# Kernel tuning notes

Measured on AMD Instinct MI355X. Metric: run time of the kernel, lower is better.

## Reference

```python
import jax, jax.numpy as jnp
import numpy as np

DIM_NODE = 128
DIM_EDGE = 128
DIM_TIME = 100
NUM_HEAD = 8
DIM_OUT = 128
LN_EPS = 1e-5


def setup_inputs() -> dict:
    key = jax.random.key(0)
    ks = jax.random.split(key, 12)
    D, E = 25000, 250000
    src_feat = jax.random.normal(ks[0], (D + E, DIM_NODE), jnp.float32)
    edge_f = jax.random.normal(ks[1], (E, DIM_EDGE), jnp.float32)
    edge_dt = jax.random.uniform(ks[2], (E,), jnp.float32)
    src_idx = jnp.arange(D + E, dtype=jnp.int64)
    edge_dst = jnp.sort(jax.random.randint(ks[3], (E,), 0, D)).astype(jnp.int64)
    # TimeEncode params (fixed init from the module)
    time_w = jnp.asarray(1.0 / 10 ** np.linspace(0, 9, DIM_TIME, dtype=np.float32))  # (DIM_TIME,)
    time_b = jnp.zeros((DIM_TIME,), jnp.float32)
    dq = DIM_NODE + DIM_TIME           # 228
    dkv = DIM_NODE + DIM_EDGE + DIM_TIME  # 356
    s = 0.05
    wq_w = jax.random.normal(ks[4], (DIM_OUT, dq), jnp.float32) * s
    wq_b = jnp.zeros((DIM_OUT,), jnp.float32)
    wk_w = jax.random.normal(ks[5], (DIM_OUT, dkv), jnp.float32) * s
    wk_b = jnp.zeros((DIM_OUT,), jnp.float32)
    wv_w = jax.random.normal(ks[6], (DIM_OUT, dkv), jnp.float32) * s
    wv_b = jnp.zeros((DIM_OUT,), jnp.float32)
    wout_w = jax.random.normal(ks[7], (DIM_OUT, DIM_NODE + DIM_OUT), jnp.float32) * s
    wout_b = jnp.zeros((DIM_OUT,), jnp.float32)
    ln_g = jnp.ones((DIM_OUT,), jnp.float32)
    ln_b = jnp.zeros((DIM_OUT,), jnp.float32)
    return dict(src_feat=src_feat, edge_f=edge_f, edge_dt=edge_dt,
                time_w=time_w, time_b=time_b,
                wq_w=wq_w, wq_b=wq_b, wk_w=wk_w, wk_b=wk_b,
                wv_w=wv_w, wv_b=wv_b, wout_w=wout_w, wout_b=wout_b,
                ln_g=ln_g, ln_b=ln_b, src_idx=src_idx, edge_dst=edge_dst)


def reference(src_feat, edge_f, edge_dt, time_w, time_b,
              wq_w, wq_b, wk_w, wk_b, wv_w, wv_b,
              wout_w, wout_b, ln_g, ln_b, src_idx, edge_dst):
    E = edge_f.shape[0]
    src_data = src_feat[src_idx]              # (D+E, dn)
    D = src_data.shape[0] - E
    q_data = src_data[:D]                     # (D, dn)
    kv_data = src_data[D:]                    # (E, dn)

    # TimeEncode: cos(w * t + b)
    time_feat = jnp.cos(edge_dt[:, None] * time_w[None, :] + time_b)       # (E, dt)
    zero_time_feat = jnp.broadcast_to(jnp.cos(time_b), (D, DIM_TIME))      # (D, dt)

    Qd = jnp.concatenate([q_data, zero_time_feat], axis=1) @ wq_w.T + wq_b  # (D, dout)
    Q = Qd[edge_dst]                                                        # (E, dout)
    kv_in = jnp.concatenate([kv_data, edge_f, time_feat], axis=1)           # (E, dkv)
    K = kv_in @ wk_w.T + wk_b
    V = kv_in @ wv_w.T + wv_b

    dh = DIM_OUT // NUM_HEAD
    Q = Q.reshape(E, NUM_HEAD, dh)
    K = K.reshape(E, NUM_HEAD, dh)
    V = V.reshape(E, NUM_HEAD, dh)

    scores = jax.nn.leaky_relu(jnp.sum(Q * K, axis=2), 0.2)   # (E, H)
    # edge softmax: segment softmax over dst nodes
    m = jax.ops.segment_max(scores, edge_dst, num_segments=D)  # (D, H)
    m = jnp.where(jnp.isfinite(m), m, 0.0)
    ex = jnp.exp(scores - m[edge_dst])
    den = jax.ops.segment_sum(ex, edge_dst, num_segments=D)    # (D, H)
    att = ex / den[edge_dst]                                    # (E, H)

    Vw = (V * att[:, :, None]).reshape(E, DIM_OUT)
    h = jax.ops.segment_sum(Vw, edge_dst, num_segments=D)       # (D, dout)

    rst = jnp.concatenate([h, q_data], axis=1) @ wout_w.T + wout_b
    rst = jax.nn.relu(rst)
    mu = jnp.mean(rst, axis=-1, keepdims=True)
    var = jnp.var(rst, axis=-1, keepdims=True)
    return (rst - mu) / jnp.sqrt(var + LN_EPS) * ln_g + ln_b
```

## Files before the change

### kernel.cpp

```cpp
#include <hip/hip_runtime.h>
#include <stdint.h>

#define DIM_TIME 100
#define DQ 228
#define DKV 356
#define KPAD 384
#define NB 256
#define BM 32
#define BK 32
#define NCHUNK 12
#define A_STRIDE 392
#define C_STRIDE 264

typedef short v8s __attribute__((ext_vector_type(8)));
typedef float v4f __attribute__((ext_vector_type(4)));

__device__ __forceinline__ unsigned short bf16_bits(float f) {
    union { float f; uint32_t u; } c; c.f = f;
    uint32_t u = c.u;
    uint32_t r = (u + 0x7FFFu + ((u >> 16) & 1u)) >> 16;
    return (unsigned short)r;
}
__device__ __forceinline__ float bf16_lo(uint32_t u) {
    union { uint32_t u; float f; } c; c.u = u << 16; return c.f;
}
__device__ __forceinline__ float bf16_hi(uint32_t u) {
    union { uint32_t u; float f; } c; c.u = u & 0xFFFF0000u; return c.f;
}

__global__ void prep_wt2(const float* __restrict__ wk_w, const float* __restrict__ wv_w,
                         unsigned short* __restrict__ Wt2) {
    int n = blockIdx.x;
    int k = threadIdx.x;
    float v = 0.f;
    if (k < DKV) v = (n < 128) ? wk_w[n * DKV + k] : wv_w[(n - 128) * DKV + k];
    Wt2[n * KPAD + k] = bf16_bits(v);
}

__global__ void prep_wqt(const float* __restrict__ wq_w, float* __restrict__ Wqt) {
    int k = blockIdx.x, o = threadIdx.x;
    Wqt[k * 128 + o] = wq_w[o * DQ + k];
}

__global__ void prep_wot(const float* __restrict__ wout_w, float* __restrict__ Wot) {
    int k = blockIdx.x, o = threadIdx.x;
    Wot[k * 128 + o] = wout_w[o * 256 + k];
}

__global__ void prep_cq(const float* __restrict__ wq_w, const float* __restrict__ wq_b,
                        const float* __restrict__ time_b, float* __restrict__ cq) {
    int o = threadIdx.x;
    float s = wq_b[o];
    for (int t = 0; t < DIM_TIME; ++t)
        s += cosf(time_b[t]) * wq_w[o * DQ + 128 + t];
    cq[o] = s;
}

__global__ __launch_bounds__(256) void qd_kernel(
        const float* __restrict__ src_feat, const int* __restrict__ src_idx,
        const float* __restrict__ Wqt, const float* __restrict__ cq,
        float* __restrict__ Qd, int D) {
    __shared__ float q_s[32][128];
    int lane = threadIdx.x & 63, wave = threadIdx.x >> 6;
    int r0 = wave * 8;
    int d0 = blockIdx.x * 32 + r0;
    #pragma unroll
    for (int i = 0; i < 8; ++i) {
        int d = d0 + i;
        float v0 = 0.f, v1 = 0.f;
        if (d < D) {
            const float* p = src_feat + (size_t)src_idx[d] * 128;
            v0 = p[lane]; v1 = p[lane + 64];
        }
        q_s[r0 + i][lane] = v0; q_s[r0 + i][lane + 64] = v1;
    }
    float2 c2 = *(const float2*)(cq + 2 * lane);
    float acc0[8], acc1[8];
    #pragma unroll
    for (int i = 0; i < 8; ++i) { acc0[i] = c2.x; acc1[i] = c2.y; }
    #pragma unroll 8
    for (int k = 0; k < 128; ++k) {
        float2 w = *(const float2*)(Wqt + k * 128 + 2 * lane);
        #pragma unroll
        for (int i = 0; i < 8; ++i) {
            float a = q_s[r0 + i][k];
            acc0[i] += a * w.x; acc1[i] += a * w.y;
        }
    }
    #pragma unroll
    for (int i = 0; i < 8; ++i) {
        int d = d0 + i;
        if (d < D)
            *(float2*)(Qd + (size_t)d * 128 + 2 * lane) = make_float2(acc0[i], acc1[i]);
    }
}

__global__ __launch_bounds__(256) void kv_mfma(
        const float* __restrict__ src_feat, const int* __restrict__ src_idx,
        const float* __restrict__ edge_f, const float* __restrict__ edge_dt,
        const float* __restrict__ time_w, const float* __restrict__ time_b,
        const unsigned short* __restrict__ Wt2,
        const float* __restrict__ wk_b, const float* __restrict__ wv_b,
        unsigned short* __restrict__ KVb, int D, int E) {
    __shared__ unsigned short A_s[BM * A_STRIDE];
    int tid = threadIdx.x;
    int e0 = blockIdx.x * BM;
    int lane = tid & 63, wave = tid >> 6;
    int l15 = lane & 15, quad = lane >> 4;
    int wn = wave * 64;

    {
        int row = tid >> 3;
        int cb  = (tid & 7) * 4;
        int e = e0 + row;
        bool ok = (e < E);
        size_t nbase = ok ? (size_t)src_idx[D + e] * 128 : 0;
        #pragma unroll
        for (int i = 0; i < 4; ++i) {
            int c4 = cb + i;
            float4 v = ok ? *(const float4*)(src_feat + nbase + c4 * 4)
                          : make_float4(0.f, 0.f, 0.f, 0.f);
            ushort4 w;
            w.x = bf16_bits(v.x); w.y = bf16_bits(v.y);
            w.z = bf16_bits(v.z); w.w = bf16_bits(v.w);
            *(ushort4*)&A_s[row * A_STRIDE + c4 * 4] = w;
        }
        #pragma unroll
        for (int i = 0; i < 4; ++i) {
            int c4 = cb + i;
            float4 v = ok ? *(const float4*)(edge_f + (size_t)e * 128 + c4 * 4)
                          : make_float4(0.f, 0.f, 0.f, 0.f);
            ushort4 w;
            w.x = bf16_bits(v.x); w.y = bf16_bits(v.y);
            w.z = bf16_bits(v.z); w.w = bf16_bits(v.w);
            *(ushort4*)&A_s[row * A_STRIDE + 128 + c4 * 4] = w;
        }
    }
    {
        int c = tid & 127;
        int rbase = tid >> 7;
        bool vc = (c < DIM_TIME);
        float tw = vc ? time_w[c] : 0.f;
        float tb = vc ? time_b[c] : 0.f;
        #pragma unroll
        for (int i = 0; i < 16; ++i) {
            int row = i * 2 + rbase;
            int e = e0 + row;
            float v = 0.f;
            if (vc && e < E) v = __cosf(edge_dt[e] * tw + tb);
            A_s[row * A_STRIDE + 256 + c] = bf16_bits(v);
        }
    }
    __syncthreads();

    v4f acc[2][4];
    #pragma unroll
    for (int mf = 0; mf < 2; ++mf)
        #pragma unroll
        for (int nf = 0; nf < 4; ++nf)
            acc[mf][nf] = (v4f)(0.f);

    const unsigned short* wp = Wt2 + (size_t)(wn + l15) * KPAD + quad * 8;
    const unsigned short* ap = A_s + l15 * A_STRIDE + quad * 8;

    v8s bcur[4], acur[2];
    #pragma unroll
    for (int nf = 0; nf < 4; ++nf) bcur[nf] = *(const v8s*)(wp + nf * 16 * KPAD);
    #pragma unroll
    for (int mf = 0; mf < 2; ++mf) acur[mf] = *(const v8s*)(ap + mf * 16 * A_STRIDE);

    #pragma unroll 2
    for (int ch = 0; ch < NCHUNK; ++ch) {
        int k2 = (ch + 1 < NCHUNK) ? (ch + 1) * BK : 0;
        v8s bn[4], an[2];
        #pragma unroll
        for (int nf = 0; nf < 4; ++nf) bn[nf] = *(const v8s*)(wp + nf * 16 * KPAD + k2);
        #pragma unroll
        for (int mf = 0; mf < 2; ++mf) an[mf] = *(const v8s*)(ap + mf * 16 * A_STRIDE + k2);
        #pragma unroll
        for (int mf = 0; mf < 2; ++mf)
            #pragma unroll
            for (int nf = 0; nf < 4; ++nf)
                acc[mf][nf] = __builtin_amdgcn_mfma_f32_16x16x32_bf16(
                                  acur[mf], bcur[nf], acc[mf][nf], 0, 0, 0);
        #pragma unroll
        for (int nf = 0; nf < 4; ++nf) bcur[nf] = bn[nf];
        #pragma unroll
        for (int mf = 0; mf < 2; ++mf) acur[mf] = an[mf];
    }

    __syncthreads();
    #pragma unroll
    for (int nf = 0; nf < 4; ++nf) {
        int n = wn + nf * 16 + l15;
        float bias = (n < 128) ? wk_b[n] : wv_b[n - 128];
        #pragma unroll
        for (int mf = 0; mf < 2; ++mf)
            #pragma unroll
            for (int r = 0; r < 4; ++r)
                A_s[(mf * 16 + quad * 4 + r) * C_STRIDE + n] =
                    bf16_bits(acc[mf][nf][r] + bias);
    }
    __syncthreads();
    #pragma unroll
    for (int j = 0; j < 4; ++j) {
        int c = j * 256 + tid;
        int row = c >> 5;
        int col = (c & 31) * 8;
        if (e0 + row < E) {
            v8s v = *(const v8s*)&A_s[row * C_STRIDE + col];
            *(v8s*)&KVb[(size_t)(e0 + row) * NB + col] = v;
        }
    }
}

__global__ void seg_offsets(const int* __restrict__ edge_dst, int* __restrict__ start,
                            int D, int E) {
    int d = blockIdx.x * blockDim.x + threadIdx.x;
    if (d > D) return;
    int lo = 0, hi = E;
    while (lo < hi) {
        int mid = (lo + hi) >> 1;
        if (edge_dst[mid] < d) lo = mid + 1; else hi = mid;
    }
    start[d] = lo;
}

__global__ __launch_bounds__(256) void attn_kernel(
        const float* __restrict__ Qd, const unsigned short* __restrict__ KVb,
        const int* __restrict__ start, float* __restrict__ h, int D) {
    int lane = threadIdx.x & 63, wave = threadIdx.x >> 6;
    int dbase = blockIdx.x * 16 + wave * 4;
    for (int i = 0; i < 4; ++i) {
        int d = dbase + i;
        if (d >= D) break;
        float2 q = *(const float2*)(Qd + (size_t)d * 128 + lane * 2);
        int s0 = start[d], s1 = start[d + 1];
        float m = -INFINITY, l = 0.f, a0 = 0.f, a1 = 0.f;
        for (int e = s0; e < s1; e += 4) {
            int n = s1 - e; if (n > 4) n = 4;
            uint32_t ku[4], vu[4];
            #pragma unroll
            for (int j = 0; j < 4; ++j) {
                if (j < n) {
                    const unsigned short* kv = KVb + (size_t)(e + j) * 256 + lane * 2;
                    ku[j] = *(const uint32_t*)kv;
                    vu[j] = *(const uint32_t*)(kv + 128);
                }
            }
            for (int j = 0; j < n; ++j) {
                float qk = q.x * bf16_lo(ku[j]) + q.y * bf16_hi(ku[j]);
                qk += __shfl_xor(qk, 4, 8);
                qk += __shfl_xor(qk, 2, 8);
                qk += __shfl_xor(qk, 1, 8);
                float s = qk > 0.f ? qk : 0.2f * qk;
                float nm = fmaxf(m, s);
                float sc = __expf(m - nm);
                float p  = __expf(s - nm);
                l  = l  * sc + p;
                a0 = a0 * sc + p * bf16_lo(vu[j]);
                a1 = a1 * sc + p * bf16_hi(vu[j]);
                m = nm;
            }
        }
        float inv = (l > 0.f) ? 1.f / l : 0.f;
        *(float2*)(h + (size_t)d * 128 + lane * 2) = make_float2(a0 * inv, a1 * inv);
    }
}

__global__ __launch_bounds__(256) void out_kernel(
        const float* __restrict__ h, const float* __restrict__ src_feat,
        const int* __restrict__ src_idx, const float* __restrict__ Wot,
        const float* __restrict__ wout_b, const float* __restrict__ ln_g,
        const float* __restrict__ ln_b, float* __restrict__ out, int D) {
    __shared__ float in_s[32][256];
    int lane = threadIdx.x & 63, wave = threadIdx.x >> 6;
    int r0 = wave * 8;
    int d0 = blockIdx.x * 32 + r0;
    #pragma unroll
    for (int i = 0; i < 8; ++i) {
        int d = d0 + i;
        float a0 = 0.f, a1 = 0.f, b0 = 0.f, b1 = 0.f;
        if (d < D) {
            const float* ph = h + (size_t)d * 128;
            a0 = ph[lane]; a1 = ph[lane + 64];
            const float* pf = src_feat + (size_t)src_idx[d] * 128;
            b0 = pf[lane]; b1 = pf[lane + 64];
        }
        in_s[r0 + i][lane] = a0; in_s[r0 + i][lane + 64] = a1;
        in_s[r0 + i][128 + lane] = b0; in_s[r0 + i][192 + lane] = b1;
    }
    float2 bb = *(const float2*)(wout_b + 2 * lane);
    float acc0[8], acc1[8];
    #pragma unroll
    for (int i = 0; i < 8; ++i) { acc0[i] = bb.x; acc1[i] = bb.y; }
    #pragma unroll 8
    for (int k = 0; k < 256; ++k) {
        float2 w = *(const float2*)(Wot + k * 128 + 2 * lane);
        #pragma unroll
        for (int i = 0; i < 8; ++i) {
            float a = in_s[r0 + i][k];
            acc0[i] += a * w.x; acc1[i] += a * w.y;
        }
    }
    float2 g = *(const float2*)(ln_g + 2 * lane);
    float2 lb = *(const float2*)(ln_b + 2 * lane);
    #pragma unroll
    for (int i = 0; i < 8; ++i) {
        float v0 = fmaxf(acc0[i], 0.f), v1 = fmaxf(acc1[i], 0.f);
        float s1 = v0 + v1, s2 = v0 * v0 + v1 * v1;
        #pragma unroll
        for (int off = 32; off; off >>= 1) {
            s1 += __shfl_xor(s1, off);
            s2 += __shfl_xor(s2, off);
        }
        float mu  = s1 * (1.f / 128.f);
        float var = s2 * (1.f / 128.f) - mu * mu;
        float rs  = rsqrtf(var + 1e-5f);
        int d = d0 + i;
        if (d < D)
            *(float2*)(out + (size_t)d * 128 + 2 * lane) =
                make_float2((v0 - mu) * rs * g.x + lb.x, (v1 - mu) * rs * g.y + lb.y);
    }
}

extern "C" void kernel_launch(void* const* d_in, const int* in_sizes, int n_in,
                              void* d_out, int out_size, void* d_ws, size_t ws_size,
                              hipStream_t stream) {
    const float* src_feat = (const float*)d_in[0];
    const float* edge_f   = (const float*)d_in[1];
    const float* edge_dt  = (const float*)d_in[2];
    const float* time_w   = (const float*)d_in[3];
    const float* time_b   = (const float*)d_in[4];
    const float* wq_w     = (const float*)d_in[5];
    const float* wq_b     = (const float*)d_in[6];
    const float* wk_w     = (const float*)d_in[7];
    const float* wk_b     = (const float*)d_in[8];
    const float* wv_w     = (const float*)d_in[9];
    const float* wv_b     = (const float*)d_in[10];
    const float* wout_w   = (const float*)d_in[11];
    const float* wout_b   = (const float*)d_in[12];
    const float* ln_g     = (const float*)d_in[13];
    const float* ln_b     = (const float*)d_in[14];
    const int*   src_idx  = (const int*)d_in[15];
    const int*   edge_dst = (const int*)d_in[16];

    int DE = in_sizes[0] / 128;
    int E  = in_sizes[1] / 128;
    int D  = DE - E;

    char* ws = (char*)d_ws;
    size_t off = 0;
    auto alloc = [&](size_t bytes) {
        void* p = ws + off;
        off = (off + bytes + 511) & ~(size_t)511;
        return p;
    };
    unsigned short* Wt2   = (unsigned short*)alloc((size_t)NB * KPAD * 2);
    float*          Wqt   = (float*)alloc(128 * 128 * 4);
    float*          Wot   = (float*)alloc(256 * 128 * 4);
    float*          cq    = (float*)alloc(128 * 4);
    float*          Qd    = (float*)alloc((size_t)D * 128 * 4);
    unsigned short* KVb   = (unsigned short*)alloc((size_t)E * 256 * 2);
    float*          hb    = (float*)alloc((size_t)D * 128 * 4);
    int*            start = (int*)alloc((size_t)(D + 1) * 4);

    hipLaunchKernelGGL(prep_wt2, dim3(NB), dim3(KPAD), 0, stream, wk_w, wv_w, Wt2);
    hipLaunchKernelGGL(prep_wqt, dim3(128), dim3(128), 0, stream, wq_w, Wqt);
    hipLaunchKernelGGL(prep_wot, dim3(256), dim3(128), 0, stream, wout_w, Wot);
    hipLaunchKernelGGL(prep_cq, dim3(1), dim3(128), 0, stream, wq_w, wq_b, time_b, cq);
    hipLaunchKernelGGL(qd_kernel, dim3((D + 31) / 32), dim3(256), 0, stream,
                       src_feat, src_idx, Wqt, cq, Qd, D);
    hipLaunchKernelGGL(kv_mfma, dim3((E + BM - 1) / BM), dim3(256), 0, stream,
                       src_feat, src_idx, edge_f, edge_dt, time_w, time_b,
                       Wt2, wk_b, wv_b, KVb, D, E);
    hipLaunchKernelGGL(seg_offsets, dim3((D + 1 + 255) / 256), dim3(256), 0, stream,
                       edge_dst, start, D, E);
    hipLaunchKernelGGL(attn_kernel, dim3((D + 15) / 16), dim3(256), 0, stream,
                       Qd, KVb, start, hb, D);
    hipLaunchKernelGGL(out_kernel, dim3((D + 31) / 32), dim3(256), 0, stream,
                       hb, src_feat, src_idx, Wot, wout_b, ln_g, ln_b, (float*)d_out, D);
}
```

Baseline: 672.8 us.

## Port Q and output projections to bf16 MFMA, stage KV weights in LDS, interleave KV

Replaces the fp32 scalar Q projection and output projection+LayerNorm kernels with bf16 MFMA versions, with weights pre-converted to bf16. The KV GEMM now stages weight chunks through LDS with register double-buffering instead of reading B fragments directly from global memory. K and V are stored interleaved per lane so attention fetches both with one 8-byte load, in batches of 8 edges and with fewer nodes per block. Trades fp32 precision in the Q/out GEMMs for bf16 and adds block barriers in the GEMM loops.

```diff
diff --git a/kernel.cpp b/kernel.cpp
--- a/kernel.cpp
+++ b/kernel.cpp
@@ -10,7 +10,13 @@
 #define BK 32
 #define NCHUNK 12
 #define A_STRIDE 392
+#define BSTR 36
 #define C_STRIDE 264
+
+#define QD_ASTR 136
+#define QD_BSTR 136
+#define OUT_ASTR 264
+#define OUT_CSTR 132
 
 typedef short v8s __attribute__((ext_vector_type(8)));
 typedef float v4f __attribute__((ext_vector_type(4)));
@@ -27,26 +33,30 @@
 __device__ __forceinline__ float bf16_hi(uint32_t u) {
     union { uint32_t u; float f; } c; c.u = u & 0xFFFF0000u; return c.f;
 }
+__device__ __forceinline__ v8s cvt8(float4 a, float4 b) {
+    union { v8s v; unsigned short u[8]; } r;
+    r.u[0] = bf16_bits(a.x); r.u[1] = bf16_bits(a.y);
+    r.u[2] = bf16_bits(a.z); r.u[3] = bf16_bits(a.w);
+    r.u[4] = bf16_bits(b.x); r.u[5] = bf16_bits(b.y);
+    r.u[6] = bf16_bits(b.z); r.u[7] = bf16_bits(b.w);
+    return r.v;
+}
 
 __global__ void prep_wt2(const float* __restrict__ wk_w, const float* __restrict__ wv_w,
                          unsigned short* __restrict__ Wt2) {
-    int n = blockIdx.x;
-    int k = threadIdx.x;
+    int n = blockIdx.x, k = threadIdx.x;
     float v = 0.f;
     if (k < DKV) v = (n < 128) ? wk_w[n * DKV + k] : wv_w[(n - 128) * DKV + k];
     Wt2[n * KPAD + k] = bf16_bits(v);
 }
-
-__global__ void prep_wqt(const float* __restrict__ wq_w, float* __restrict__ Wqt) {
-    int k = blockIdx.x, o = threadIdx.x;
-    Wqt[k * 128 + o] = wq_w[o * DQ + k];
-}
-
-__global__ void prep_wot(const float* __restrict__ wout_w, float* __restrict__ Wot) {
-    int k = blockIdx.x, o = threadIdx.x;
-    Wot[k * 128 + o] = wout_w[o * 256 + k];
-}
-
+__global__ void prep_wqb(const float* __restrict__ wq_w, unsigned short* __restrict__ Wqb) {
+    int n = blockIdx.x, k = threadIdx.x;
+    Wqb[n * 128 + k] = bf16_bits(wq_w[n * DQ + k]);
+}
+__global__ void prep_wob(const float* __restrict__ wout_w, unsigned short* __restrict__ Wob) {
+    int n = blockIdx.x, k = threadIdx.x;
+    Wob[n * 256 + k] = bf16_bits(wout_w[n * 256 + k]);
+}
 __global__ void prep_cq(const float* __restrict__ wq_w, const float* __restrict__ wq_b,
                         const float* __restrict__ time_b, float* __restrict__ cq) {
     int o = threadIdx.x;
@@ -56,42 +66,78 @@
     cq[o] = s;
 }
 
-__global__ __launch_bounds__(256) void qd_kernel(
+__global__ __launch_bounds__(256) void qd_mfma(
         const float* __restrict__ src_feat, const int* __restrict__ src_idx,
-        const float* __restrict__ Wqt, const float* __restrict__ cq,
+        const unsigned short* __restrict__ Wqb, const float* __restrict__ cq,
         float* __restrict__ Qd, int D) {
-    __shared__ float q_s[32][128];
-    int lane = threadIdx.x & 63, wave = threadIdx.x >> 6;
-    int r0 = wave * 8;
-    int d0 = blockIdx.x * 32 + r0;
-    #pragma unroll
-    for (int i = 0; i < 8; ++i) {
-        int d = d0 + i;
-        float v0 = 0.f, v1 = 0.f;
-        if (d < D) {
-            const float* p = src_feat + (size_t)src_idx[d] * 128;
-            v0 = p[lane]; v1 = p[lane + 64];
-        }
-        q_s[r0 + i][lane] = v0; q_s[r0 + i][lane + 64] = v1;
-    }
-    float2 c2 = *(const float2*)(cq + 2 * lane);
-    float acc0[8], acc1[8];
-    #pragma unroll
-    for (int i = 0; i < 8; ++i) { acc0[i] = c2.x; acc1[i] = c2.y; }
-    #pragma unroll 8
-    for (int k = 0; k < 128; ++k) {
-        float2 w = *(const float2*)(Wqt + k * 128 + 2 * lane);
-        #pragma unroll
-        for (int i = 0; i < 8; ++i) {
-            float a = q_s[r0 + i][k];
-            acc0[i] += a * w.x; acc1[i] += a * w.y;
-        }
-    }
-    #pragma unroll
-    for (int i = 0; i < 8; ++i) {
-        int d = d0 + i;
-        if (d < D)
-            *(float2*)(Qd + (size_t)d * 128 + 2 * lane) = make_float2(acc0[i], acc1[i]);
+    __shared__ unsigned short A_s[32 * QD_ASTR];
+    __shared__ unsigned short B_s[128 * QD_BSTR];
+    int tid = threadIdx.x;
+    int lane = tid & 63, wave = tid >> 6;
+    int l15 = lane & 15, quad = lane >> 4;
+    int wn = wave * 32;
+    int d0 = blockIdx.x * 32;
+
+    {
+        int row = tid >> 2, sub = tid & 3;
+        #pragma unroll
+        for (int j = 0; j < 2; ++j) {
+            int r = row + j * 64;
+            #pragma unroll
+            for (int t = 0; t < 4; ++t) {
+                v8s v = *(const v8s*)(Wqb + (size_t)r * 128 + sub * 32 + t * 8);
+                *(v8s*)&B_s[r * QD_BSTR + sub * 32 + t * 8] = v;
+            }
+        }
+    }
+    {
+        int row = tid >> 3, sub = tid & 7;
+        int d = d0 + row;
+        bool ok = (d < D);
+        size_t base = ok ? (size_t)src_idx[d] * 128 : 0;
+        float4 z = make_float4(0.f, 0.f, 0.f, 0.f);
+        float4 f0 = ok ? *(const float4*)(src_feat + base + sub * 16)      : z;
+        float4 f1 = ok ? *(const float4*)(src_feat + base + sub * 16 + 4)  : z;
+        float4 f2 = ok ? *(const float4*)(src_feat + base + sub * 16 + 8)  : z;
+        float4 f3 = ok ? *(const float4*)(src_feat + base + sub * 16 + 12) : z;
+        *(v8s*)&A_s[row * QD_ASTR + sub * 16]     = cvt8(f0, f1);
+        *(v8s*)&A_s[row * QD_ASTR + sub * 16 + 8] = cvt8(f2, f3);
+    }
+    __syncthreads();
+
+    v4f acc[2][2];
+    #pragma unroll
+    for (int mf = 0; mf < 2; ++mf)
+        #pragma unroll
+        for (int nf = 0; nf < 2; ++nf) acc[mf][nf] = (v4f)(0.f);
+
+    #pragma unroll
+    for (int ch = 0; ch < 4; ++ch) {
+        v8s af[2], bf[2];
+        #pragma unroll
+        for (int mf = 0; mf < 2; ++mf)
+            af[mf] = *(const v8s*)&A_s[(mf * 16 + l15) * QD_ASTR + ch * 32 + quad * 8];
+        #pragma unroll
+        for (int nf = 0; nf < 2; ++nf)
+            bf[nf] = *(const v8s*)&B_s[(wn + nf * 16 + l15) * QD_BSTR + ch * 32 + quad * 8];
+        #pragma unroll
+        for (int mf = 0; mf < 2; ++mf)
+            #pragma unroll
+            for (int nf = 0; nf < 2; ++nf)
+                acc[mf][nf] = __builtin_amdgcn_mfma_f32_16x16x32_bf16(
+                                  af[mf], bf[nf], acc[mf][nf], 0, 0, 0);
+    }
+    #pragma unroll
+    for (int nf = 0; nf < 2; ++nf) {
+        int n = wn + nf * 16 + l15;
+        float b = cq[n];
+        #pragma unroll
+        for (int mf = 0; mf < 2; ++mf)
+            #pragma unroll
+            for (int r = 0; r < 4; ++r) {
+                int d = d0 + mf * 16 + quad * 4 + r;
+                if (d < D) Qd[(size_t)d * 128 + n] = acc[mf][nf][r] + b;
+            }
     }
 }
 
@@ -103,37 +149,37 @@
         const float* __restrict__ wk_b, const float* __restrict__ wv_b,
         unsigned short* __restrict__ KVb, int D, int E) {
     __shared__ unsigned short A_s[BM * A_STRIDE];
+    __shared__ unsigned short B_s[NB * BSTR];
     int tid = threadIdx.x;
     int e0 = blockIdx.x * BM;
     int lane = tid & 63, wave = tid >> 6;
     int l15 = lane & 15, quad = lane >> 4;
     int wn = wave * 64;
+    int srow = tid >> 2, ssub = tid & 3;
+    const unsigned short* wsrc = Wt2 + (size_t)srow * KPAD + ssub * 8;
+
+    v8s breg[4];
+    #pragma unroll
+    for (int j = 0; j < 4; ++j)
+        breg[j] = *(const v8s*)(wsrc + (size_t)j * 64 * KPAD);
 
     {
-        int row = tid >> 3;
-        int cb  = (tid & 7) * 4;
+        int row = tid >> 3, cb = (tid & 7) * 4;
         int e = e0 + row;
         bool ok = (e < E);
         size_t nbase = ok ? (size_t)src_idx[D + e] * 128 : 0;
-        #pragma unroll
-        for (int i = 0; i < 4; ++i) {
-            int c4 = cb + i;
-            float4 v = ok ? *(const float4*)(src_feat + nbase + c4 * 4)
-                          : make_float4(0.f, 0.f, 0.f, 0.f);
-            ushort4 w;
-            w.x = bf16_bits(v.x); w.y = bf16_bits(v.y);
-            w.z = bf16_bits(v.z); w.w = bf16_bits(v.w);
-            *(ushort4*)&A_s[row * A_STRIDE + c4 * 4] = w;
-        }
-        #pragma unroll
-        for (int i = 0; i < 4; ++i) {
-            int c4 = cb + i;
-            float4 v = ok ? *(const float4*)(edge_f + (size_t)e * 128 + c4 * 4)
-                          : make_float4(0.f, 0.f, 0.f, 0.f);
-            ushort4 w;
-            w.x = bf16_bits(v.x); w.y = bf16_bits(v.y);
-            w.z = bf16_bits(v.z); w.w = bf16_bits(v.w);
-            *(ushort4*)&A_s[row * A_STRIDE + 128 + c4 * 4] = w;
+        float4 z = make_float4(0.f, 0.f, 0.f, 0.f);
+        #pragma unroll
+        for (int i = 0; i < 4; i += 2) {
+            float4 a = ok ? *(const float4*)(src_feat + nbase + (cb + i) * 4)     : z;
+            float4 b = ok ? *(const float4*)(src_feat + nbase + (cb + i + 1) * 4) : z;
+            *(v8s*)&A_s[row * A_STRIDE + (cb + i) * 4] = cvt8(a, b);
+        }
+        #pragma unroll
+        for (int i = 0; i < 4; i += 2) {
+            float4 a = ok ? *(const float4*)(edge_f + (size_t)e * 128 + (cb + i) * 4)     : z;
+            float4 b = ok ? *(const float4*)(edge_f + (size_t)e * 128 + (cb + i + 1) * 4) : z;
+            *(v8s*)&A_s[row * A_STRIDE + 128 + (cb + i) * 4] = cvt8(a, b);
         }
     }
     {
@@ -152,53 +198,60 @@
         }
     }
     __syncthreads();
+    #pragma unroll
+    for (int j = 0; j < 4; ++j)
+        *(v8s*)&B_s[(srow + j * 64) * BSTR + ssub * 8] = breg[j];
+    #pragma unroll
+    for (int j = 0; j < 4; ++j)
+        breg[j] = *(const v8s*)(wsrc + (size_t)j * 64 * KPAD + BK);
+    __syncthreads();
 
     v4f acc[2][4];
     #pragma unroll
     for (int mf = 0; mf < 2; ++mf)
         #pragma unroll
+        for (int nf = 0; nf < 4; ++nf) acc[mf][nf] = (v4f)(0.f);
+
+    for (int ch = 0; ch < NCHUNK; ++ch) {
+        v8s af[2], bf[4];
+        #pragma unroll
+        for (int mf = 0; mf < 2; ++mf)
+            af[mf] = *(const v8s*)&A_s[(mf * 16 + l15) * A_STRIDE + ch * BK + quad * 8];
+        #pragma unroll
         for (int nf = 0; nf < 4; ++nf)
-            acc[mf][nf] = (v4f)(0.f);
-
-    const unsigned short* wp = Wt2 + (size_t)(wn + l15) * KPAD + quad * 8;
-    const unsigned short* ap = A_s + l15 * A_STRIDE + quad * 8;
-
-    v8s bcur[4], acur[2];
-    #pragma unroll
-    for (int nf = 0; nf < 4; ++nf) bcur[nf] = *(const v8s*)(wp + nf * 16 * KPAD);
-    #pragma unroll
-    for (int mf = 0; mf < 2; ++mf) acur[mf] = *(const v8s*)(ap + mf * 16 * A_STRIDE);
-
-    #pragma unroll 2
-    for (int ch = 0; ch < NCHUNK; ++ch) {
-        int k2 = (ch + 1 < NCHUNK) ? (ch + 1) * BK : 0;
-        v8s bn[4], an[2];
-        #pragma unroll
-        for (int nf = 0; nf < 4; ++nf) bn[nf] = *(const v8s*)(wp + nf * 16 * KPAD + k2);
-        #pragma unroll
-        for (int mf = 0; mf < 2; ++mf) an[mf] = *(const v8s*)(ap + mf * 16 * A_STRIDE + k2);
+            bf[nf] = *(const v8s*)&B_s[(wn + nf * 16 + l15) * BSTR + quad * 8];
         #pragma unroll
         for (int mf = 0; mf < 2; ++mf)
             #pragma unroll
             for (int nf = 0; nf < 4; ++nf)
                 acc[mf][nf] = __builtin_amdgcn_mfma_f32_16x16x32_bf16(
-                                  acur[mf], bcur[nf], acc[mf][nf], 0, 0, 0);
-        #pragma unroll
-        for (int nf = 0; nf < 4; ++nf) bcur[nf] = bn[nf];
-        #pragma unroll
-        for (int mf = 0; mf < 2; ++mf) acur[mf] = an[mf];
+                                  af[mf], bf[nf], acc[mf][nf], 0, 0, 0);
+        if (ch + 1 < NCHUNK) {
+            __syncthreads();
+            #pragma unroll
+            for (int j = 0; j < 4; ++j)
+                *(v8s*)&B_s[(srow + j * 64) * BSTR + ssub * 8] = breg[j];
+            if (ch + 2 < NCHUNK) {
+                #pragma unroll
+                for (int j = 0; j < 4; ++j)
+                    breg[j] = *(const v8s*)(wsrc + (size_t)j * 64 * KPAD + (ch + 2) * BK);
+            }
+            __syncthreads();
+        }
     }
 
     __syncthreads();
     #pragma unroll
     for (int nf = 0; nf < 4; ++nf) {
         int n = wn + nf * 16 + l15;
-        float bias = (n < 128) ? wk_b[n] : wv_b[n - 128];
+        float bias; int slot;
+        if (n < 128) { bias = wk_b[n]; slot = 2 * n - (n & 1); }
+        else { int m = n - 128; bias = wv_b[m]; slot = 2 * m + 2 - (m & 1); }
         #pragma unroll
         for (int mf = 0; mf < 2; ++mf)
             #pragma unroll
             for (int r = 0; r < 4; ++r)
-                A_s[(mf * 16 + quad * 4 + r) * C_STRIDE + n] =
+                A_s[(mf * 16 + quad * 4 + r) * C_STRIDE + slot] =
                     bf16_bits(acc[mf][nf][r] + bias);
     }
     __syncthreads();
@@ -230,26 +283,25 @@
         const float* __restrict__ Qd, const unsigned short* __restrict__ KVb,
         const int* __restrict__ start, float* __restrict__ h, int D) {
     int lane = threadIdx.x & 63, wave = threadIdx.x >> 6;
-    int dbase = blockIdx.x * 16 + wave * 4;
-    for (int i = 0; i < 4; ++i) {
+    int dbase = blockIdx.x * 8 + wave * 2;
+    #pragma unroll
+    for (int i = 0; i < 2; ++i) {
         int d = dbase + i;
-        if (d >= D) break;
+        if (d >= D) continue;
         float2 q = *(const float2*)(Qd + (size_t)d * 128 + lane * 2);
         int s0 = start[d], s1 = start[d + 1];
         float m = -INFINITY, l = 0.f, a0 = 0.f, a1 = 0.f;
-        for (int e = s0; e < s1; e += 4) {
-            int n = s1 - e; if (n > 4) n = 4;
-            uint32_t ku[4], vu[4];
-            #pragma unroll
-            for (int j = 0; j < 4; ++j) {
-                if (j < n) {
-                    const unsigned short* kv = KVb + (size_t)(e + j) * 256 + lane * 2;
-                    ku[j] = *(const uint32_t*)kv;
-                    vu[j] = *(const uint32_t*)(kv + 128);
-                }
+        for (int e = s0; e < s1; e += 8) {
+            int n = s1 - e; if (n > 8) n = 8;
+            uint2 w8[8];
+            #pragma unroll
+            for (int j = 0; j < 8; ++j) {
+                int idx = e + j; if (idx >= s1) idx = s1 - 1;
+                w8[j] = *(const uint2*)(KVb + (size_t)idx * 256 + lane * 4);
             }
             for (int j = 0; j < n; ++j) {
-                float qk = q.x * bf16_lo(ku[j]) + q.y * bf16_hi(ku[j]);
+                uint32_t ku = w8[j].x, vu = w8[j].y;
+                float qk = q.x * bf16_lo(ku) + q.y * bf16_hi(ku);
                 qk += __shfl_xor(qk, 4, 8);
                 qk += __shfl_xor(qk, 2, 8);
                 qk += __shfl_xor(qk, 1, 8);
@@ -258,8 +310,8 @@
                 float sc = __expf(m - nm);
                 float p  = __expf(s - nm);
                 l  = l  * sc + p;
-                a0 = a0 * sc + p * bf16_lo(vu[j]);
-                a1 = a1 * sc + p * bf16_hi(vu[j]);
+                a0 = a0 * sc + p * bf16_lo(vu);
+                a1 = a1 * sc + p * bf16_hi(vu);
                 m = nm;
             }
         }
@@ -268,59 +320,148 @@
     }
 }
 
-__global__ __launch_bounds__(256) void out_kernel(
+__global__ __launch_bounds__(256) void out_mfma(
         const float* __restrict__ h, const float* __restrict__ src_feat,
-        const int* __restrict__ src_idx, const float* __restrict__ Wot,
+        const int* __restrict__ src_idx, const unsigned short* __restrict__ Wob,
         const float* __restrict__ wout_b, const float* __restrict__ ln_g,
         const float* __restrict__ ln_b, float* __restrict__ out, int D) {
-    __shared__ float in_s[32][256];
-    int lane = threadIdx.x & 63, wave = threadIdx.x >> 6;
-    int r0 = wave * 8;
-    int d0 = blockIdx.x * 32 + r0;
-    #pragma unroll
-    for (int i = 0; i < 8; ++i) {
-        int d = d0 + i;
-        float a0 = 0.f, a1 = 0.f, b0 = 0.f, b1 = 0.f;
-        if (d < D) {
-            const float* ph = h + (size_t)d * 128;
-            a0 = ph[lane]; a1 = ph[lane + 64];
-            const float* pf = src_feat + (size_t)src_idx[d] * 128;
-            b0 = pf[lane]; b1 = pf[lane + 64];
-        }
-        in_s[r0 + i][lane] = a0; in_s[r0 + i][lane + 64] = a1;
-        in_s[r0 + i][128 + lane] = b0; in_s[r0 + i][192 + lane] = b1;
-    }
-    float2 bb = *(const float2*)(wout_b + 2 * lane);
-    float acc0[8], acc1[8];
-    #pragma unroll
-    for (int i = 0; i < 8; ++i) { acc0[i] = bb.x; acc1[i] = bb.y; }
-    #pragma unroll 8
-    for (int k = 0; k < 256; ++k) {
-        float2 w = *(const float2*)(Wot + k * 128 + 2 * lane);
-        #pragma unroll
-        for (int i = 0; i < 8; ++i) {
-            float a = in_s[r0 + i][k];
-            acc0[i] += a * w.x; acc1[i] += a * w.y;
-        }
-    }
-    float2 g = *(const float2*)(ln_g + 2 * lane);
-    float2 lb = *(const float2*)(ln_b + 2 * lane);
-    #pragma unroll
-    for (int i = 0; i < 8; ++i) {
-        float v0 = fmaxf(acc0[i], 0.f), v1 = fmaxf(acc1[i], 0.f);
-        float s1 = v0 + v1, s2 = v0 * v0 + v1 * v1;
-        #pragma unroll
-        for (int off = 32; off; off >>= 1) {
-            s1 += __shfl_xor(s1, off);
-            s2 += __shfl_xor(s2, off);
-        }
+    __shared__ unsigned short A_s[32 * OUT_ASTR];
+    __shared__ unsigned short B_s[128 * BSTR];
+    __shared__ float C_s[32 * OUT_CSTR];
+    int tid = threadIdx.x;
+    int lane = tid & 63, wave = tid >> 6;
+    int l15 = lane & 15, quad = lane >> 4;
+    int wn = wave * 32;
+    int d0 = blockIdx.x * 32;
+    int srow = tid >> 2, ssub = tid & 3;
+    const unsigned short* wsrc = Wob + (size_t)srow * 256 + ssub * 8;
+
+    v8s breg[2];
+    #pragma unroll
+    for (int j = 0; j < 2; ++j)
+        breg[j] = *(const v8s*)(wsrc + (size_t)j * 64 * 256);
+
+    {
+        int row = tid >> 3, sub = tid & 7;
+        int d = d0 + row;
+        bool ok = (d < D);
+        const float* src = (sub < 4) ? (ok ? h + (size_t)d * 128 + sub * 32 : h)
+                                     : (ok ? src_feat + (size_t)src_idx[d] * 128 + (sub - 4) * 32
+                                           : src_feat);
+        float4 z = make_float4(0.f, 0.f, 0.f, 0.f);
+        float4 f0 = ok ? *(const float4*)(src)      : z;
+        float4 f1 = ok ? *(const float4*)(src + 4)  : z;
+        float4 f2 = ok ? *(const float4*)(src + 8)  : z;
+        float4 f3 = ok ? *(const float4*)(src + 12) : z;
+        float4 f4 = ok ? *(const float4*)(src + 16) : z;
+        float4 f5 = ok ? *(const float4*)(src + 20) : z;
+        float4 f6 = ok ? *(const float4*)(src + 24) : z;
+        float4 f7 = ok ? *(const float4*)(src + 28) : z;
+        *(v8s*)&A_s[row * OUT_ASTR + sub * 32]      = cvt8(f0, f1);
+        *(v8s*)&A_s[row * OUT_ASTR + sub * 32 + 8]  = cvt8(f2, f3);
+        *(v8s*)&A_s[row * OUT_ASTR + sub * 32 + 16] = cvt8(f4, f5);
+        *(v8s*)&A_s[row * OUT_ASTR + sub * 32 + 24] = cvt8(f6, f7);
+    }
+    __syncthreads();
+    #pragma unroll
+    for (int j = 0; j < 2; ++j)
+        *(v8s*)&B_s[(srow + j * 64) * BSTR + ssub * 8] = breg[j];
+    #pragma unroll
+    for (int j = 0; j < 2; ++j)
+        breg[j] = *(const v8s*)(wsrc + (size_t)j * 64 * 256 + BK);
+    __syncthreads();
+
+    v4f acc[2][2];
+    #pragma unroll
+    for (int mf = 0; mf < 2; ++mf)
+        #pragma unroll
+        for (int nf = 0; nf < 2; ++nf) acc[mf][nf] = (v4f)(0.f);
+
+    for (int ch = 0; ch < 8; ++ch) {
+        v8s af[2], bf[2];
+        #pragma unroll
+        for (int mf = 0; mf < 2; ++mf)
+            af[mf] = *(const v8s*)&A_s[(mf * 16 + l15) * OUT_ASTR + ch * BK + quad * 8];
+        #pragma unroll
+        for (int nf = 0; nf < 2; ++nf)
+            bf[nf] = *(const v8s*)&B_s[(wn + nf * 16 + l15) * BSTR + quad * 8];
+        #pragma unroll
+        for (int mf = 0; mf < 2; ++mf)
+            #pragma unroll
+            for (int nf = 0; nf < 2; ++nf)
+                acc[mf][nf] = __builtin_amdgcn_mfma_f32_16x16x32_bf16(
+                                  af[mf], bf[nf], acc[mf][nf], 0, 0, 0);
+        if (ch + 1 < 8) {
+            __syncthreads();
+            #pragma unroll
+            for (int j = 0; j < 2; ++j)
+                *(v8s*)&B_s[(srow + j * 64) * BSTR + ssub * 8] = breg[j];
+            if (ch + 2 < 8) {
+                #pragma unroll
+                for (int j = 0; j < 2; ++j)
+                    breg[j] = *(const v8s*)(wsrc + (size_t)j * 64 * 256 + (ch + 2) * BK);
+            }
+            __syncthreads();
+        }
+    }
+
+    __syncthreads();
+    #pragma unroll
+    for (int nf = 0; nf < 2; ++nf) {
+        int n = wn + nf * 16 + l15;
+        float b = wout_b[n];
+        #pragma unroll
+        for (int mf = 0; mf < 2; ++mf)
+            #pragma unroll
+            for (int r = 0; r < 4; ++r)
+                C_s[(mf * 16 + quad * 4 + r) * OUT_CSTR + n] =
+                    fmaxf(acc[mf][nf][r] + b, 0.f);
+    }
+    __syncthreads();
+
+    {
+        int row = tid >> 3, s = tid & 7;
+        const float* cr = C_s + row * OUT_CSTR + s * 16;
+        float4 x0 = *(const float4*)(cr);
+        float4 x1 = *(const float4*)(cr + 4);
+        float4 x2 = *(const float4*)(cr + 8);
+        float4 x3 = *(const float4*)(cr + 12);
+        float s1 = x0.x+x0.y+x0.z+x0.w + x1.x+x1.y+x1.z+x1.w
+                 + x2.x+x2.y+x2.z+x2.w + x3.x+x3.y+x3.z+x3.w;
+        float s2 = x0.x*x0.x+x0.y*x0.y+x0.z*x0.z+x0.w*x0.w
+                 + x1.x*x1.x+x1.y*x1.y+x1.z*x1.z+x1.w*x1.w
+                 + x2.x*x2.x+x2.y*x2.y+x2.z*x2.z+x2.w*x2.w
+                 + x3.x*x3.x+x3.y*x3.y+x3.z*x3.z+x3.w*x3.w;
+        s1 += __shfl_xor(s1, 4, 8); s2 += __shfl_xor(s2, 4, 8);
+        s1 += __shfl_xor(s1, 2, 8); s2 += __shfl_xor(s2, 2, 8);
+        s1 += __shfl_xor(s1, 1, 8); s2 += __shfl_xor(s2, 1, 8);
         float mu  = s1 * (1.f / 128.f);
         float var = s2 * (1.f / 128.f) - mu * mu;
         float rs  = rsqrtf(var + 1e-5f);
-        int d = d0 + i;
-        if (d < D)
-            *(float2*)(out + (size_t)d * 128 + 2 * lane) =
-                make_float2((v0 - mu) * rs * g.x + lb.x, (v1 - mu) * rs * g.y + lb.y);
+        int d = d0 + row;
+        if (d < D) {
+            float4 g0 = *(const float4*)(ln_g + s * 16);
+            float4 g1 = *(const float4*)(ln_g + s * 16 + 4);
+            float4 g2 = *(const float4*)(ln_g + s * 16 + 8);
+            float4 g3 = *(const float4*)(ln_g + s * 16 + 12);
+            float4 b0 = *(const float4*)(ln_b + s * 16);
+            float4 b1 = *(const float4*)(ln_b + s * 16 + 4);
+            float4 b2 = *(const float4*)(ln_b + s * 16 + 8);
+            float4 b3 = *(const float4*)(ln_b + s * 16 + 12);
+            float* op = out + (size_t)d * 128 + s * 16;
+            float4 o0 = make_float4((x0.x-mu)*rs*g0.x+b0.x, (x0.y-mu)*rs*g0.y+b0.y,
+                                    (x0.z-mu)*rs*g0.z+b0.z, (x0.w-mu)*rs*g0.w+b0.w);
+            float4 o1 = make_float4((x1.x-mu)*rs*g1.x+b1.x, (x1.y-mu)*rs*g1.y+b1.y,
+                                    (x1.z-mu)*rs*g1.z+b1.z, (x1.w-mu)*rs*g1.w+b1.w);
+            float4 o2 = make_float4((x2.x-mu)*rs*g2.x+b2.x, (x2.y-mu)*rs*g2.y+b2.y,
+                                    (x2.z-mu)*rs*g2.z+b2.z, (x2.w-mu)*rs*g2.w+b2.w);
+            float4 o3 = make_float4((x3.x-mu)*rs*g3.x+b3.x, (x3.y-mu)*rs*g3.y+b3.y,
+                                    (x3.z-mu)*rs*g3.z+b3.z, (x3.w-mu)*rs*g3.w+b3.w);
+            *(float4*)(op)      = o0;
+            *(float4*)(op + 4)  = o1;
+            *(float4*)(op + 8)  = o2;
+            *(float4*)(op + 12) = o3;
+        }
     }
 }
 
@@ -357,8 +498,8 @@
         return p;
     };
     unsigned short* Wt2   = (unsigned short*)alloc((size_t)NB * KPAD * 2);
-    float*          Wqt   = (float*)alloc(128 * 128 * 4);
-    float*          Wot   = (float*)alloc(256 * 128 * 4);
+    unsigned short* Wqb   = (unsigned short*)alloc(128 * 128 * 2);
+    unsigned short* Wob   = (unsigned short*)alloc(128 * 256 * 2);
     float*          cq    = (float*)alloc(128 * 4);
     float*          Qd    = (float*)alloc((size_t)D * 128 * 4);
     unsigned short* KVb   = (unsigned short*)alloc((size_t)E * 256 * 2);
@@ -366,18 +507,18 @@
     int*            start = (int*)alloc((size_t)(D + 1) * 4);
 
     hipLaunchKernelGGL(prep_wt2, dim3(NB), dim3(KPAD), 0, stream, wk_w, wv_w, Wt2);
-    hipLaunchKernelGGL(prep_wqt, dim3(128), dim3(128), 0, stream, wq_w, Wqt);
-    hipLaunchKernelGGL(prep_wot, dim3(256), dim3(128), 0, stream, wout_w, Wot);
+    hipLaunchKernelGGL(prep_wqb, dim3(128), dim3(128), 0, stream, wq_w, Wqb);
+    hipLaunchKernelGGL(prep_wob, dim3(128), dim3(256), 0, stream, wout_w, Wob);
     hipLaunchKernelGGL(prep_cq, dim3(1), dim3(128), 0, stream, wq_w, wq_b, time_b, cq);
-    hipLaunchKernelGGL(qd_kernel, dim3((D + 31) / 32), dim3(256), 0, stream,
-                       src_feat, src_idx, Wqt, cq, Qd, D);
+    hipLaunchKernelGGL(qd_mfma, dim3((D + 31) / 32), dim3(256), 0, stream,
+                       src_feat, src_idx, Wqb, cq, Qd, D);
     hipLaunchKernelGGL(kv_mfma, dim3((E + BM - 1) / BM), dim3(256), 0, stream,
                        src_feat, src_idx, edge_f, edge_dt, time_w, time_b,
                        Wt2, wk_b, wv_b, KVb, D, E);
     hipLaunchKernelGGL(seg_offsets, dim3((D + 1 + 255) / 256), dim3(256), 0, stream,
                        edge_dst, start, D, E);
-    hipLaunchKernelGGL(attn_kernel, dim3((D + 15) / 16), dim3(256), 0, stream,
+    hipLaunchKernelGGL(attn_kernel, dim3((D + 7) / 8), dim3(256), 0, stream,
                        Qd, KVb, start, hb, D);
-    hipLaunchKernelGGL(out_kernel, dim3((D + 31) / 32), dim3(256), 0, stream,
-                       hb, src_feat, src_idx, Wot, wout_b, ln_g, ln_b, (float*)d_out, D);
-}
+    hipLaunchKernelGGL(out_mfma, dim3((D + 31) / 32), dim3(256), 0, stream,
+                       hb, src_feat, src_idx, Wob, wout_b, ln_g, ln_b, (float*)d_out, D);
+}
```

Measured after the change: 613.1 us. -8.9%, faster.
